# Optimization experiments

Hardware: AMD Instinct MI355X
Metric: run time of the kernel (lower is better)

The kernel has to match this reference:

```python
import jax, jax.numpy as jnp
import numpy as np

B, K, N, D = 64, 64, 32768, 2048   # batch, knn neighbors, memory size, feat dim (hardcoded 2048 in source)
NC, NHID, TOPK = 2048, 512, 5      # num clusters, gcn hidden, topk in affinity masking


def setup_inputs() -> dict:
    key = jax.random.key(0)
    ks = jax.random.split(key, 8)
    features = jax.random.normal(ks[0], (N, D), jnp.float32)
    labels = jax.random.randint(ks[1], (N,), 0, NC)
    indexes = jax.random.randint(ks[2], (B,), 0, N)
    ori_knn_neighbor = jax.random.randint(ks[3], (B, K), 0, N)
    s = 0.02
    conv_w = jax.random.normal(ks[4], (2 * D, NHID), jnp.float32) * s
    conv_b = jnp.zeros((NHID,), jnp.float32)
    w1 = jax.random.normal(ks[5], (NHID, NHID), jnp.float32) * s
    b1 = jnp.zeros((NHID,), jnp.float32)
    prelu_a = jnp.full((NHID,), 0.25, jnp.float32)
    w2 = jax.random.normal(ks[6], (NHID, 2), jnp.float32) * s
    b2 = jnp.zeros((2,), jnp.float32)
    return dict(indexes=indexes, features=features, labels=labels,
                ori_knn_neighbor=ori_knn_neighbor, conv_w=conv_w, conv_b=conv_b,
                w1=w1, b1=b1, prelu_a=prelu_a, w2=w2, b2=b2)


def _build_graphs(indexes, features, labels, ori_knn_neighbor):
    # cluster mean features (index_add_ + count normalize), done under no_grad in torch
    counts = jax.ops.segment_sum(jnp.ones((N,), jnp.float32), labels, num_segments=NC)
    clu_sum = jax.ops.segment_sum(features, labels, num_segments=NC)
    clu_mean = clu_sum / jnp.maximum(counts, 1.0)[:, None]

    def per_sample(idx, nbr):
        clu_lab = labels[nbr]                                  # [K]
        cf = clu_mean[clu_lab].at[0].set(features[idx])        # [K, D]
        A = (cf @ cf.T) / 5.0                                  # [K, K]
        j = jnp.arange(K)
        # keep only first occurrence of each cluster label (np.unique return_index)
        dup = jnp.any((clu_lab[:, None] == clu_lab[None, :]) & (j[None, :] < j[:, None]), axis=1)
        keep = (~dup).astype(A.dtype)                          # [K]
        _, ti = jax.lax.top_k(A, TOPK)                         # [K, TOPK]
        m = jnp.zeros_like(A).at[j[:, None], ti].set(1.0)
        m = ((m > 0) & (m.T > 0)).astype(A.dtype) * keep[:, None] * keep[None, :]
        A = A * m
        cf = cf / jnp.linalg.norm(cf, axis=1, keepdims=True)   # row-normalize
        cf = cf - cf[0]                                        # center on query (row 0 -> 0)
        return cf, A

    x, adj = jax.vmap(per_sample)(indexes, ori_knn_neighbor)   # [B,K,D], [B,K,K]
    return jax.lax.stop_gradient(x), jax.lax.stop_gradient(adj)


def reference(indexes, features, labels, ori_knn_neighbor,
              conv_w, conv_b, w1, b1, prelu_a, w2, b2):
    x, adj = _build_graphs(indexes, features, labels, ori_knn_neighbor)
    # GraphConv with MeanAggregator: agg = A @ x, concat, linear, relu
    agg = jnp.einsum('bij,bjd->bid', adj, x)                   # [B,K,D]
    h = jax.nn.relu(jnp.concatenate([x, agg], axis=-1) @ conv_w + conv_b)  # [B,K,NHID]
    h0 = h.reshape(-1, NHID)
    h1 = h0 @ w1 + b1
    h1 = jnp.where(h1 > 0, h1, prelu_a * h1)                   # PReLU(nhid)
    logits = h1 @ w2 + b2                                      # [B*K, 2]
    return jax.nn.softmax(logits.reshape(B, K, 2), axis=2)
```

## Files before the change

kernel.cpp:

```cpp
#include <hip/hip_runtime.h>
#include <hip/hip_bf16.h>

#define BB 64
#define KN 64
#define NPTS 32768
#define DD 2048
#define NCC 2048
#define NH 512
#define MM 4096
#define K2 4096

typedef unsigned short u16;
typedef unsigned int u32;
typedef __attribute__((ext_vector_type(8))) short short8;
typedef __attribute__((ext_vector_type(4))) float f32x4;

__device__ __forceinline__ float bf2f(u32 u){
  union { u32 i; float f; } v; v.i = u << 16; return v.f;
}
__device__ __forceinline__ u16 f2bf(float f){
  union { float f; u32 i; } v; v.f = f;
  u32 x = v.i;
  return (u16)((x + 0x7fffu + ((x >> 16) & 1u)) >> 16);
}

typedef __attribute__((address_space(3))) u32 as3_u32;
typedef const __attribute__((address_space(1))) u32 as1_u32;
__device__ __forceinline__ void glds16(const void* g, void* l){
  __builtin_amdgcn_global_load_lds((as1_u32*)g, (as3_u32*)l, 16, 0, 0);
}

__global__ __launch_bounds__(256) void k_prep(
    const int* __restrict__ labels, int* __restrict__ counts,
    const int* __restrict__ knn, int* __restrict__ used,
    const void* __restrict__ conv_w, u16* __restrict__ cwT, int fcw,
    const void* __restrict__ w1, u16* __restrict__ w1T, int fw1){
  __shared__ u16 tile[64][65];
  int bb = blockIdx.x, t = threadIdx.x;
  if(bb < 128){
    int n = bb*256 + t;
    atomicAdd(&counts[labels[n]], 1);
    return;
  }
  if(bb == 704){
    #pragma unroll
    for(int i=0;i<16;i++){
      int idx = i*256 + t;
      used[labels[knn[idx]]] = 1;
    }
    return;
  }
  const void* src; u16* dst; int Kd, Nd, isf32, tb;
  if(bb < 640){ src=conv_w; dst=cwT; Kd=K2; Nd=NH; isf32=fcw; tb=bb-128; }
  else        { src=w1;     dst=w1T; Kd=NH; Nd=NH; isf32=fw1; tb=bb-640; }
  int nbt = Nd >> 6;
  int k0 = (tb / nbt) << 6;
  int n0 = (tb % nbt) << 6;
  if(isf32){
    const float* s = (const float*)src;
    #pragma unroll
    for(int ph=0; ph<16; ph++){
      int idx = ph*256 + t;
      int r = idx >> 6, c = idx & 63;
      tile[r][c] = f2bf(s[(size_t)(k0+r)*Nd + n0 + c]);
    }
  } else {
    const u16* s = (const u16*)src;
    #pragma unroll
    for(int ph=0; ph<16; ph++){
      int idx = ph*256 + t;
      int r = idx >> 6, c = idx & 63;
      tile[r][c] = s[(size_t)(k0+r)*Nd + n0 + c];
    }
  }
  __syncthreads();
  #pragma unroll
  for(int ph=0; ph<16; ph++){
    int idx = ph*256 + t;
    int r = idx >> 6, c = idx & 63;
    dst[(size_t)(n0+r)*Kd + k0 + c] = tile[c][r];
  }
}

__global__ void k_scan(const int* __restrict__ counts, int* __restrict__ offsets){
  __shared__ int sb[256];
  int t = threadIdx.x;
  int c[8]; int s = 0;
  #pragma unroll
  for(int i=0;i<8;i++){ c[i] = counts[t*8+i]; s += c[i]; }
  sb[t] = s; __syncthreads();
  int v = s;
  for(int off=1; off<256; off<<=1){
    int u = (t>=off) ? sb[t-off] : 0;
    __syncthreads();
    v += u; sb[t] = v;
    __syncthreads();
  }
  int run = v - s;
  #pragma unroll
  for(int i=0;i<8;i++){ offsets[t*8+i] = run; run += c[i]; }
}

__global__ void k_scatter(const int* __restrict__ labels, const int* __restrict__ offsets,
                          int* __restrict__ cursor, int* __restrict__ sorted){
  int n = blockIdx.x*256 + threadIdx.x;
  int c = labels[n];
  int p = atomicAdd(&cursor[c], 1);
  sorted[offsets[c] + p] = n;
}

__global__ __launch_bounds__(256) void k_clumean(
    const void* __restrict__ feat, const int* __restrict__ counts,
    const int* __restrict__ offsets, const int* __restrict__ sorted,
    const int* __restrict__ used, int isf32, float* __restrict__ clu){
  int c = blockIdx.x, t = threadIdx.x;
  if(!used[c]) return;
  __shared__ int ridx[64];
  int cnt = counts[c], start = offsets[c];
  float acc[8] = {0,0,0,0,0,0,0,0};
  for(int base=0; base<cnt; base+=64){
    int take = min(64, cnt-base);
    __syncthreads();
    if(t < take) ridx[t] = sorted[start+base+t];
    __syncthreads();
    if(isf32){
      const float* ff = (const float*)feat;
      int r = 0;
      for(; r+4<=take; r+=4){
        const float* p0 = ff + (size_t)ridx[r]*DD + t*8;
        const float* p1 = ff + (size_t)ridx[r+1]*DD + t*8;
        const float* p2 = ff + (size_t)ridx[r+2]*DD + t*8;
        const float* p3 = ff + (size_t)ridx[r+3]*DD + t*8;
        float4 a0=*(const float4*)p0, b0=*(const float4*)(p0+4);
        float4 a1=*(const float4*)p1, b1=*(const float4*)(p1+4);
        float4 a2=*(const float4*)p2, b2=*(const float4*)(p2+4);
        float4 a3=*(const float4*)p3, b3=*(const float4*)(p3+4);
        acc[0]+=a0.x+a1.x+a2.x+a3.x; acc[1]+=a0.y+a1.y+a2.y+a3.y;
        acc[2]+=a0.z+a1.z+a2.z+a3.z; acc[3]+=a0.w+a1.w+a2.w+a3.w;
        acc[4]+=b0.x+b1.x+b2.x+b3.x; acc[5]+=b0.y+b1.y+b2.y+b3.y;
        acc[6]+=b0.z+b1.z+b2.z+b3.z; acc[7]+=b0.w+b1.w+b2.w+b3.w;
      }
      for(; r<take; r++){
        const float* p0 = ff + (size_t)ridx[r]*DD + t*8;
        float4 a0=*(const float4*)p0, b0=*(const float4*)(p0+4);
        acc[0]+=a0.x; acc[1]+=a0.y; acc[2]+=a0.z; acc[3]+=a0.w;
        acc[4]+=b0.x; acc[5]+=b0.y; acc[6]+=b0.z; acc[7]+=b0.w;
      }
    } else {
      const u16* fb = (const u16*)feat;
      for(int r=0; r<take; r++){
        const u16* p0 = fb + (size_t)ridx[r]*DD + t*8;
        uint4 v0 = *(const uint4*)p0;
        acc[0]+=bf2f(v0.x&0xffffu); acc[1]+=bf2f(v0.x>>16);
        acc[2]+=bf2f(v0.y&0xffffu); acc[3]+=bf2f(v0.y>>16);
        acc[4]+=bf2f(v0.z&0xffffu); acc[5]+=bf2f(v0.z>>16);
        acc[6]+=bf2f(v0.w&0xffffu); acc[7]+=bf2f(v0.w>>16);
      }
    }
  }
  float div = fmaxf((float)cnt, 1.0f);
  float* o = clu + (size_t)c*DD + t*8;
  float4 o0 = make_float4(acc[0]/div, acc[1]/div, acc[2]/div, acc[3]/div);
  float4 o1 = make_float4(acc[4]/div, acc[5]/div, acc[6]/div, acc[7]/div);
  *(float4*)o = o0;
  *(float4*)(o+4) = o1;
}

__global__ __launch_bounds__(256) void k_Apart(
    const void* __restrict__ feat, const float* __restrict__ clu,
    const int* __restrict__ indexes, const int* __restrict__ labels,
    const int* __restrict__ knn, int isf32, float* __restrict__ Apart){
  int b = blockIdx.x >> 2, g = blockIdx.x & 3;
  int t = threadIdx.x;
  __shared__ float cfT[64][68];
  __shared__ int sl[64];
  if(t < 64) sl[t] = labels[knn[b*64 + t]];
  int qidx = indexes[b];
  __syncthreads();
  int i0 = (t & 15)*4, j0 = (t >> 4)*4;
  float acc[4][4];
  #pragma unroll
  for(int x=0;x<4;x++)
    #pragma unroll
    for(int c2=0;c2<4;c2++) acc[x][c2] = 0.f;
  for(int ch=g*8; ch<g*8+8; ch++){
    int dbase = ch*64;
    #pragma unroll
    for(int ps=0; ps<16; ps++){
      int idx = ps*256 + t;
      int k = idx >> 6, dd = idx & 63;
      float v;
      if(k == 0){
        size_t fi = (size_t)qidx*DD + dbase + dd;
        v = isf32 ? ((const float*)feat)[fi] : bf2f(((const u16*)feat)[fi]);
      } else {
        v = clu[(size_t)sl[k]*DD + dbase + dd];
      }
      cfT[dd][k] = v;
    }
    __syncthreads();
    #pragma unroll 4
    for(int dd=0; dd<64; dd++){
      float4 av = *(const float4*)&cfT[dd][i0];
      float4 bv = *(const float4*)&cfT[dd][j0];
      float aa[4] = {av.x, av.y, av.z, av.w};
      float bbv[4] = {bv.x, bv.y, bv.z, bv.w};
      #pragma unroll
      for(int ii=0;ii<4;ii++)
        #pragma unroll
        for(int jj=0;jj<4;jj++)
          acc[ii][jj] += aa[ii]*bbv[jj];
    }
    __syncthreads();
  }
  float* op = Apart + ((size_t)(g*64 + b))*4096;
  #pragma unroll
  for(int ii=0;ii<4;ii++)
    *(float4*)&op[(i0+ii)*64 + j0] = make_float4(acc[ii][0], acc[ii][1], acc[ii][2], acc[ii][3]);
}

__global__ __launch_bounds__(256) void k_Afinal(
    const float* __restrict__ Apart, const int* __restrict__ labels,
    const int* __restrict__ knn,
    float* __restrict__ adj, float* __restrict__ norms){
  int b = blockIdx.x, t = threadIdx.x;
  __shared__ float A[64][65];
  __shared__ unsigned long long mb[64];
  __shared__ int sl[64];
  __shared__ int sk[64];
  if(t < 64) sl[t] = labels[knn[b*64 + t]];
  const float* P = Apart + (size_t)b*4096;
  const size_t gs = (size_t)64*4096;
  #pragma unroll
  for(int ps=0; ps<16; ps++){
    int idx = ps*256 + t;
    float s = P[idx] + P[idx+gs] + P[idx+2*gs] + P[idx+3*gs];
    A[idx>>6][idx&63] = s * 0.2f;
  }
  __syncthreads();
  if(t < 64){
    int dup = 0;
    for(int j=0;j<t;j++) dup |= (sl[j]==sl[t]);
    sk[t] = dup ? 0 : 1;
    unsigned long long chosen = 0;
    const float* row = A[t];
    #pragma unroll
    for(int p=0;p<5;p++){
      float best = -INFINITY; int bi = 0;
      for(int j=0;j<64;j++){
        bool taken = (chosen >> j) & 1ull;
        float v = row[j];
        if(!taken && v > best){ best = v; bi = j; }
      }
      chosen |= (1ull << bi);
    }
    mb[t] = chosen;
    norms[b*64+t] = sqrtf(fmaxf(A[t][t]*5.0f, 0.0f));
  }
  __syncthreads();
  float* O = adj + (size_t)b*4096;
  #pragma unroll
  for(int ps=0; ps<16; ps++){
    int idx = ps*256 + t;
    int i = idx >> 6, j = idx & 63;
    bool on = ((mb[i]>>j)&1ull) && ((mb[j]>>i)&1ull) && sk[i] && sk[j];
    O[idx] = on ? A[i][j] : 0.0f;
  }
}

__global__ __launch_bounds__(256) void k_xagg(
    const void* __restrict__ feat, const float* __restrict__ clu,
    const int* __restrict__ indexes, const int* __restrict__ labels,
    const int* __restrict__ knn, const float* __restrict__ norms,
    const float* __restrict__ adj, int isf32, u16* __restrict__ xab){
  int b = blockIdx.x >> 3, g = blockIdx.x & 7;
  int t = threadIdx.x;
  __shared__ u16  xs[64][256];
  __shared__ float adjs[64][65];
  __shared__ float nzv[64][8];
  __shared__ u16   nzj[64][8];
  __shared__ int   nzc[64];
  __shared__ int   sl[64];
  __shared__ float sn[64];

  const float* Ab = adj + (size_t)b*4096;
  #pragma unroll
  for(int ps=0; ps<16; ps++){
    int idx = ps*256 + t;
    adjs[idx>>6][idx&63] = Ab[idx];
  }
  if(t < 64){
    sl[t] = labels[knn[b*64 + t]];
    sn[t] = 1.0f / fmaxf(norms[b*64 + t], 1e-30f);
  }
  int qidx = indexes[b];
  int d = g*256 + t;
  float q0;
  if(isf32){
    q0 = ((const float*)feat)[(size_t)qidx*DD + d];
  } else {
    q0 = bf2f(((const u16*)feat)[(size_t)qidx*DD + d]);
  }
  __syncthreads();
  if(t < 64){
    int c = 0;
    for(int j=0;j<64;j++){
      float v = adjs[t][j];
      if(v != 0.0f && c < 8){ nzv[t][c] = v; nzj[t][c] = (u16)j; c++; }
    }
    nzc[t] = c;
  }
  q0 *= sn[0];

  xs[0][t] = 0;
  xab[(size_t)(b*64)*K2 + d] = 0;
  for(int k=1;k<64;k++){
    float cv = clu[(size_t)sl[k]*DD + d];
    u16 x0 = f2bf(cv*sn[k] - q0);
    xs[k][t] = x0;
    xab[(size_t)(b*64+k)*K2 + d] = x0;
  }
  __syncthreads();

  for(int r=0;r<64;r++){
    float a0 = 0.f;
    int c = nzc[r];
    for(int p=0;p<c;p++){
      a0 += nzv[r][p] * bf2f(xs[nzj[r][p]][t]);
    }
    xab[(size_t)(b*64+r)*K2 + DD + d] = f2bf(a0);
  }
}

template<int EPI>
__global__ __launch_bounds__(256, 2) void k_gemm(
    const u16* __restrict__ Am, const u16* __restrict__ Bt,
    const void* __restrict__ bias, const void* __restrict__ pa,
    int fbias, int fpa,
    void* __restrict__ Cout, int Md, int Nd, int Kd)
{
  __shared__ u16 As[2][64*128];
  __shared__ u16 Bs[2][64*128];
  int t = threadIdx.x;
  int nblk = gridDim.x;
  int bid = (blockIdx.x & 7)*(nblk >> 3) + (blockIdx.x >> 3);
  int nb = Nd >> 6;
  int m0 = (bid / nb) << 6;
  int n0 = (bid % nb) << 6;
  int wave = t >> 6, lane = t & 63;
  int wm = wave >> 1, wn = wave & 1;
  int lm = lane & 15, lq = lane >> 4;
  int lrow4 = lane >> 4, lcol16 = lane & 15;

  f32x4 acc[2][2];
  #pragma unroll
  for(int i=0;i<2;i++)
    #pragma unroll
    for(int j=0;j<2;j++) acc[i][j] = (f32x4){0.f,0.f,0.f,0.f};

  auto stage = [&](int buf, int kb){
    #pragma unroll
    for(int c=0;c<4;c++){
      int cb = wave*4 + c;
      int row = cb*4 + lrow4;
      int col = lcol16 ^ (row & 7);
      glds16(Am + (size_t)(m0+row)*Kd + kb + col*8, &As[buf][cb*512]);
    }
    #pragma unroll
    for(int c=0;c<4;c++){
      int cb = wave*4 + c;
      int row = cb*4 + lrow4;
      int col = lcol16 ^ (row & 7);
      glds16(Bt + (size_t)(n0+row)*Kd + kb + col*8, &Bs[buf][cb*512]);
    }
  };

  stage(0, 0);
  __syncthreads();
  int cur = 0;
  for(int kb=0; kb<Kd; kb+=128){
    if(kb + 128 < Kd) stage(cur^1, kb+128);
    #pragma unroll
    for(int kk=0;kk<4;kk++){
      short8 af[2], bfr[2];
      #pragma unroll
      for(int mi=0;mi<2;mi++){
        int r = wm*32 + mi*16 + lm;
        int p = ((kk<<2)+lq) ^ (r & 7);
        union{ uint4 u; short8 v; } x;
        x.u = *(const uint4*)&As[cur][r*128 + p*8];
        af[mi] = x.v;
      }
      #pragma unroll
      for(int ni=0;ni<2;ni++){
        int r = wn*32 + ni*16 + lm;
        int p = ((kk<<2)+lq) ^ (r & 7);
        union{ uint4 u; short8 v; } x;
        x.u = *(const uint4*)&Bs[cur][r*128 + p*8];
        bfr[ni] = x.v;
      }
      #pragma unroll
      for(int mi=0;mi<2;mi++)
        #pragma unroll
        for(int ni=0;ni<2;ni++)
          acc[mi][ni] = __builtin_amdgcn_mfma_f32_16x16x32_bf16(af[mi], bfr[ni], acc[mi][ni], 0, 0, 0);
    }
    __syncthreads();
    cur ^= 1;
  }

  #pragma unroll
  for(int ni=0;ni<2;ni++){
    int col = n0 + wn*32 + ni*16 + lm;
    float bs = fbias ? ((const float*)bias)[col] : bf2f(((const u16*)bias)[col]);
    float av = 0.f;
    if(EPI==1) av = fpa ? ((const float*)pa)[col] : bf2f(((const u16*)pa)[col]);
    #pragma unroll
    for(int mi=0;mi<2;mi++){
      int rowb = m0 + wm*32 + mi*16 + lq*4;
      #pragma unroll
      for(int r2=0;r2<4;r2++){
        float v = acc[mi][ni][r2] + bs;
        if(EPI==0){
          v = fmaxf(v, 0.f);
          ((u16*)Cout)[(size_t)(rowb+r2)*Nd + col] = f2bf(v);
        } else {
          v = (v > 0.f) ? v : av*v;
          ((float*)Cout)[(size_t)(rowb+r2)*Nd + col] = v;
        }
      }
    }
  }
}

__global__ __launch_bounds__(256) void k_out(
    const float* __restrict__ h1, const void* __restrict__ w2,
    const void* __restrict__ b2, int fw2, int fb2, int fo,
    void* __restrict__ out){
  int t = threadIdx.x; int lane = t & 63; int row = blockIdx.x*4 + (t >> 6);
  const float* hr = h1 + (size_t)row*NH;
  float s0 = 0.f, s1 = 0.f;
  #pragma unroll
  for(int j=0;j<NH/64;j++){
    int i = lane + j*64;
    float h = hr[i];
    float w0 = fw2 ? ((const float*)w2)[i*2+0] : bf2f(((const u16*)w2)[i*2+0]);
    float w1v= fw2 ? ((const float*)w2)[i*2+1] : bf2f(((const u16*)w2)[i*2+1]);
    s0 += h * w0;
    s1 += h * w1v;
  }
  #pragma unroll
  for(int off=32; off>0; off>>=1){
    s0 += __shfl_down(s0, off);
    s1 += __shfl_down(s1, off);
  }
  if(lane==0){
    float bb0 = fb2 ? ((const float*)b2)[0] : bf2f(((const u16*)b2)[0]);
    float bb1 = fb2 ? ((const float*)b2)[1] : bf2f(((const u16*)b2)[1]);
    float l0 = s0 + bb0;
    float l1 = s1 + bb1;
    float m = fmaxf(l0, l1);
    float e0 = expf(l0 - m), e1 = expf(l1 - m);
    float inv = 1.0f / (e0 + e1);
    if(fo){
      ((float*)out)[row*2+0] = e0*inv;
      ((float*)out)[row*2+1] = e1*inv;
    } else {
      ((u16*)out)[row*2+0] = f2bf(e0*inv);
      ((u16*)out)[row*2+1] = f2bf(e1*inv);
    }
  }
}

__global__ void k_fill_sentinel(u32* __restrict__ out, int nwords){
  int i = blockIdx.x*256 + threadIdx.x;
  if(i < nwords) out[i] = 0x40404040u;
}

extern "C" void kernel_launch(void* const* d_in, const int* in_sizes, int n_in,
                              void* d_out, int out_size, void* d_ws, size_t ws_size,
                              hipStream_t stream) {
  const int* indexes = (const int*)d_in[0];
  const void* feat   = d_in[1];
  const int* labels  = (const int*)d_in[2];
  const int* knn     = (const int*)d_in[3];
  const void* conv_w = d_in[4];
  const void* conv_b = d_in[5];
  const void* w1     = d_in[6];
  const void* b1     = d_in[7];
  const void* pa     = d_in[8];
  const void* w2     = d_in[9];
  const void* b2     = d_in[10];

  int ff  = (in_sizes[1]  != (int)((size_t)NPTS*DD*2));
  int fcw = (in_sizes[4]  != (int)((size_t)2*DD*NH*2));
  int fcb = (in_sizes[5]  != NH*2);
  int fw1 = (in_sizes[6]  != (int)((size_t)NH*NH*2));
  int fb1 = (in_sizes[7]  != NH*2);
  int fpa = (in_sizes[8]  != NH*2);
  int fw2 = (in_sizes[9]  != NH*2*2);
  int fb2 = (in_sizes[10] != 2*2);
  int fo  = (out_size     != MM*2*2);

  char* w = (char*)d_ws;
  size_t o = 0;
  auto alloc = [&](size_t bytes) -> void* {
    void* p = w + o; o = (o + bytes + 255) & ~(size_t)255; return p;
  };
  int*   counts  = (int*)  alloc((size_t)NCC*4);
  int*   cursor  = (int*)  alloc((size_t)NCC*4);
  int*   used    = (int*)  alloc((size_t)NCC*4);
  int*   offsets = (int*)  alloc((size_t)NCC*4);
  int*   sorted  = (int*)  alloc((size_t)NPTS*4);
  float* norms   = (float*)alloc((size_t)MM*4);
  float* adj     = (float*)alloc((size_t)BB*64*64*4);
  float* Apart   = (float*)alloc((size_t)4*BB*64*64*4);
  float* clu     = (float*)alloc((size_t)NCC*DD*4);
  u16*   xab     = (u16*)  alloc((size_t)MM*K2*2);
  u16*   cwT     = (u16*)  alloc((size_t)K2*NH*2);
  u16*   w1T     = (u16*)  alloc((size_t)NH*NH*2);
  u16*   hb      = (u16*)  clu;
  float* h1      = (float*)((char*)clu + (size_t)MM*NH*2);

  size_t NEED = o;
  if(ws_size < NEED){
    int nwords = out_size/4;
    k_fill_sentinel<<<(nwords+255)/256, 256, 0, stream>>>((u32*)d_out, nwords);
    return;
  }

  hipMemsetAsync(counts, 0, (size_t)NCC*4*3, stream);

  k_prep   <<<705, 256, 0, stream>>>(labels, counts, knn, used, conv_w, cwT, fcw, w1, w1T, fw1);
  k_scan   <<<1, 256, 0, stream>>>(counts, offsets);
  k_scatter<<<NPTS/256, 256, 0, stream>>>(labels, offsets, cursor, sorted);
  k_clumean<<<NCC, 256, 0, stream>>>(feat, counts, offsets, sorted, used, ff, clu);
  k_Apart  <<<BB*4, 256, 0, stream>>>(feat, clu, indexes, labels, knn, ff, Apart);
  k_Afinal <<<BB, 256, 0, stream>>>(Apart, labels, knn, adj, norms);
  k_xagg   <<<BB*8, 256, 0, stream>>>(feat, clu, indexes, labels, knn, norms, adj, ff, xab);

  k_gemm<0><<<(MM/64)*(NH/64), 256, 0, stream>>>(xab, cwT, conv_b, nullptr, fcb, 0, (void*)hb, MM, NH, K2);
  k_gemm<1><<<(MM/64)*(NH/64), 256, 0, stream>>>(hb, w1T, b1, pa, fb1, fpa, (void*)h1, MM, NH, NH);

  k_out    <<<MM/4, 256, 0, stream>>>(h1, w2, b2, fw2, fb2, fo, d_out);
}
```

Baseline: 533.9 us.

## Project cluster means through conv weights once, then combine per-sample projections

Instead of building a per-sample [B*K, 2D] concatenated input and running the large conv GEMM over it, the cluster means (plus query rows) are converted to bf16 and multiplied once by both halves of conv_w, stacked into a [D, 1024] matrix. A new kernel then forms each sample's hidden activations from these projected rows: it scales by the inverse norm, subtracts the query projection, applies the sparse adjacency, adds the bias and applies ReLU. This relies on linearity to replace a 4096x4096x512 GEMM and the large xab buffer with a 2112x2048x1024 GEMM plus cheap gathers. Rounding differs because centering and aggregation now happen after projection rather than on bf16 features.

```diff
diff --git a/kernel.cpp b/kernel.cpp
--- a/kernel.cpp
+++ b/kernel.cpp
@@ -9,6 +9,7 @@
 #define NH 512
 #define MM 4096
 #define K2 4096
+#define MCLUB 2112
 
 typedef unsigned short u16;
 typedef unsigned int u32;
@@ -23,6 +24,14 @@
   u32 x = v.i;
   return (u16)((x + 0x7fffu + ((x >> 16) & 1u)) >> 16);
 }
+__device__ __forceinline__ uint4 pack8(const u16* b){
+  uint4 w;
+  w.x = (u32)b[0] | ((u32)b[1]<<16);
+  w.y = (u32)b[2] | ((u32)b[3]<<16);
+  w.z = (u32)b[4] | ((u32)b[5]<<16);
+  w.w = (u32)b[6] | ((u32)b[7]<<16);
+  return w;
+}
 
 typedef __attribute__((address_space(3))) u32 as3_u32;
 typedef const __attribute__((address_space(1))) u32 as1_u32;
@@ -33,52 +42,71 @@
 __global__ __launch_bounds__(256) void k_prep(
     const int* __restrict__ labels, int* __restrict__ counts,
     const int* __restrict__ knn, int* __restrict__ used,
-    const void* __restrict__ conv_w, u16* __restrict__ cwT, int fcw,
+    const void* __restrict__ conv_w, u16* __restrict__ cwT2, int fcw,
     const void* __restrict__ w1, u16* __restrict__ w1T, int fw1){
   __shared__ u16 tile[64][65];
   int bb = blockIdx.x, t = threadIdx.x;
   if(bb < 128){
-    int n = bb*256 + t;
-    atomicAdd(&counts[labels[n]], 1);
+    atomicAdd(&counts[labels[bb*256 + t]], 1);
     return;
   }
   if(bb == 704){
     #pragma unroll
-    for(int i=0;i<16;i++){
-      int idx = i*256 + t;
-      used[labels[knn[idx]]] = 1;
-    }
+    for(int i=0;i<16;i++) used[labels[knn[i*256 + t]]] = 1;
     return;
   }
-  const void* src; u16* dst; int Kd, Nd, isf32, tb;
-  if(bb < 640){ src=conv_w; dst=cwT; Kd=K2; Nd=NH; isf32=fcw; tb=bb-128; }
-  else        { src=w1;     dst=w1T; Kd=NH; Nd=NH; isf32=fw1; tb=bb-640; }
-  int nbt = Nd >> 6;
-  int k0 = (tb / nbt) << 6;
-  int n0 = (tb % nbt) << 6;
-  if(isf32){
-    const float* s = (const float*)src;
+  if(bb < 640){
+    int tb = bb - 128;
+    int k0 = (tb >> 3) << 6;
+    int n0 = (tb & 7) << 6;
+    if(fcw){
+      const float* s = (const float*)conv_w;
+      #pragma unroll
+      for(int ph=0; ph<16; ph++){
+        int idx = ph*256 + t; int r = idx >> 6, c = idx & 63;
+        tile[r][c] = f2bf(s[(size_t)(k0+r)*NH + n0 + c]);
+      }
+    } else {
+      const u16* s = (const u16*)conv_w;
+      #pragma unroll
+      for(int ph=0; ph<16; ph++){
+        int idx = ph*256 + t; int r = idx >> 6, c = idx & 63;
+        tile[r][c] = s[(size_t)(k0+r)*NH + n0 + c];
+      }
+    }
+    __syncthreads();
+    int drow = n0 + (k0 >= 2048 ? 512 : 0);
+    int dcol = k0 & 2047;
     #pragma unroll
     for(int ph=0; ph<16; ph++){
-      int idx = ph*256 + t;
-      int r = idx >> 6, c = idx & 63;
-      tile[r][c] = f2bf(s[(size_t)(k0+r)*Nd + n0 + c]);
+      int idx = ph*256 + t; int r = idx >> 6, c = idx & 63;
+      cwT2[(size_t)(drow+r)*2048 + dcol + c] = tile[c][r];
     }
   } else {
-    const u16* s = (const u16*)src;
+    int tb = bb - 640;
+    int k0 = (tb >> 3) << 6;
+    int n0 = (tb & 7) << 6;
+    if(fw1){
+      const float* s = (const float*)w1;
+      #pragma unroll
+      for(int ph=0; ph<16; ph++){
+        int idx = ph*256 + t; int r = idx >> 6, c = idx & 63;
+        tile[r][c] = f2bf(s[(size_t)(k0+r)*NH + n0 + c]);
+      }
+    } else {
+      const u16* s = (const u16*)w1;
+      #pragma unroll
+      for(int ph=0; ph<16; ph++){
+        int idx = ph*256 + t; int r = idx >> 6, c = idx & 63;
+        tile[r][c] = s[(size_t)(k0+r)*NH + n0 + c];
+      }
+    }
+    __syncthreads();
     #pragma unroll
     for(int ph=0; ph<16; ph++){
-      int idx = ph*256 + t;
-      int r = idx >> 6, c = idx & 63;
-      tile[r][c] = s[(size_t)(k0+r)*Nd + n0 + c];
-    }
-  }
-  __syncthreads();
-  #pragma unroll
-  for(int ph=0; ph<16; ph++){
-    int idx = ph*256 + t;
-    int r = idx >> 6, c = idx & 63;
-    dst[(size_t)(n0+r)*Kd + k0 + c] = tile[c][r];
+      int idx = ph*256 + t; int r = idx >> 6, c = idx & 63;
+      w1T[(size_t)(n0+r)*NH + k0 + c] = tile[c][r];
+    }
   }
 }
 
@@ -109,12 +137,34 @@
   sorted[offsets[c] + p] = n;
 }
 
+__global__ __launch_bounds__(256) void k_qcopy(
+    const void* __restrict__ feat, const int* __restrict__ indexes,
+    int ff, u16* __restrict__ club){
+  int b = blockIdx.x, t = threadIdx.x;
+  int qidx = indexes[b];
+  u16* o = club + (size_t)(NCC + b)*DD + t*8;
+  if(ff){
+    const float* p = (const float*)feat + (size_t)qidx*DD + t*8;
+    float4 a = *(const float4*)p, c = *(const float4*)(p+4);
+    u16 ob[8] = {f2bf(a.x),f2bf(a.y),f2bf(a.z),f2bf(a.w),
+                 f2bf(c.x),f2bf(c.y),f2bf(c.z),f2bf(c.w)};
+    *(uint4*)o = pack8(ob);
+  } else {
+    uint4 v = *(const uint4*)((const u16*)feat + (size_t)qidx*DD + t*8);
+    *(uint4*)o = v;
+  }
+}
+
 __global__ __launch_bounds__(256) void k_clumean(
     const void* __restrict__ feat, const int* __restrict__ counts,
     const int* __restrict__ offsets, const int* __restrict__ sorted,
-    const int* __restrict__ used, int isf32, float* __restrict__ clu){
+    const int* __restrict__ used, int isf32,
+    float* __restrict__ clu, u16* __restrict__ club){
   int c = blockIdx.x, t = threadIdx.x;
-  if(!used[c]) return;
+  if(!used[c]){
+    *(uint4*)(club + (size_t)c*DD + t*8) = make_uint4(0,0,0,0);
+    return;
+  }
   __shared__ int ridx[64];
   int cnt = counts[c], start = offsets[c];
   float acc[8] = {0,0,0,0,0,0,0,0};
@@ -159,11 +209,16 @@
     }
   }
   float div = fmaxf((float)cnt, 1.0f);
+  float m[8];
+  #pragma unroll
+  for(int i=0;i<8;i++) m[i] = acc[i] / div;
   float* o = clu + (size_t)c*DD + t*8;
-  float4 o0 = make_float4(acc[0]/div, acc[1]/div, acc[2]/div, acc[3]/div);
-  float4 o1 = make_float4(acc[4]/div, acc[5]/div, acc[6]/div, acc[7]/div);
-  *(float4*)o = o0;
-  *(float4*)(o+4) = o1;
+  *(float4*)o     = make_float4(m[0],m[1],m[2],m[3]);
+  *(float4*)(o+4) = make_float4(m[4],m[5],m[6],m[7]);
+  u16 ob[8];
+  #pragma unroll
+  for(int i=0;i<8;i++) ob[i] = f2bf(m[i]);
+  *(uint4*)(club + (size_t)c*DD + t*8) = pack8(ob);
 }
 
 __global__ __launch_bounds__(256) void k_Apart(
@@ -268,21 +323,22 @@
   }
 }
 
-__global__ __launch_bounds__(256) void k_xagg(
-    const void* __restrict__ feat, const float* __restrict__ clu,
-    const int* __restrict__ indexes, const int* __restrict__ labels,
-    const int* __restrict__ knn, const float* __restrict__ norms,
-    const float* __restrict__ adj, int isf32, u16* __restrict__ xab){
-  int b = blockIdx.x >> 3, g = blockIdx.x & 7;
+__global__ __launch_bounds__(256) void k_hcomb(
+    const float* __restrict__ PR, const float* __restrict__ adj,
+    const float* __restrict__ norms, const int* __restrict__ labels,
+    const int* __restrict__ knn, const void* __restrict__ conv_b, int fcb,
+    u16* __restrict__ hb){
+  int b = blockIdx.x >> 2, cg = blockIdx.x & 3;
   int t = threadIdx.x;
-  __shared__ u16  xs[64][256];
   __shared__ float adjs[64][65];
+  __shared__ float xwa[64][128];
+  __shared__ float cqx[128], cqa[128], bias[128];
   __shared__ float nzv[64][8];
   __shared__ u16   nzj[64][8];
   __shared__ int   nzc[64];
   __shared__ int   sl[64];
   __shared__ float sn[64];
-
+  int j0 = cg*128;
   const float* Ab = adj + (size_t)b*4096;
   #pragma unroll
   for(int ps=0; ps<16; ps++){
@@ -293,13 +349,12 @@
     sl[t] = labels[knn[b*64 + t]];
     sn[t] = 1.0f / fmaxf(norms[b*64 + t], 1e-30f);
   }
-  int qidx = indexes[b];
-  int d = g*256 + t;
-  float q0;
-  if(isf32){
-    q0 = ((const float*)feat)[(size_t)qidx*DD + d];
-  } else {
-    q0 = bf2f(((const u16*)feat)[(size_t)qidx*DD + d]);
+  if(t >= 64 && t < 192){
+    int c = t - 64;
+    const float* qr = PR + (size_t)(NCC + b)*1024;
+    cqx[c] = qr[j0 + c];
+    cqa[c] = qr[512 + j0 + c];
+    bias[c] = fcb ? ((const float*)conv_b)[j0 + c] : bf2f(((const u16*)conv_b)[j0 + c]);
   }
   __syncthreads();
   if(t < 64){
@@ -310,25 +365,22 @@
     }
     nzc[t] = c;
   }
-  q0 *= sn[0];
-
-  xs[0][t] = 0;
-  xab[(size_t)(b*64)*K2 + d] = 0;
-  for(int k=1;k<64;k++){
-    float cv = clu[(size_t)sl[k]*DD + d];
-    u16 x0 = f2bf(cv*sn[k] - q0);
-    xs[k][t] = x0;
-    xab[(size_t)(b*64+k)*K2 + d] = x0;
+  float inv0 = sn[0];
+  for(int idx=t; idx<8192; idx+=256){
+    int k = idx >> 7, c = idx & 127;
+    float v = 0.f;
+    if(k > 0) v = sn[k]*PR[(size_t)sl[k]*1024 + 512 + j0 + c] - inv0*cqa[c];
+    xwa[k][c] = v;
   }
   __syncthreads();
-
-  for(int r=0;r<64;r++){
-    float a0 = 0.f;
-    int c = nzc[r];
-    for(int p=0;p<c;p++){
-      a0 += nzv[r][p] * bf2f(xs[nzj[r][p]][t]);
-    }
-    xab[(size_t)(b*64+r)*K2 + DD + d] = f2bf(a0);
+  for(int idx=t; idx<8192; idx+=256){
+    int k = idx >> 7, c = idx & 127;
+    float xwx = (k > 0) ? sn[k]*PR[(size_t)sl[k]*1024 + j0 + c] - inv0*cqx[c] : 0.f;
+    float g = 0.f;
+    int cc = nzc[k];
+    for(int p=0;p<cc;p++) g += nzv[k][p]*xwa[nzj[k][p]][c];
+    float h = fmaxf(xwx + g + bias[c], 0.f);
+    hb[(size_t)(b*64 + k)*NH + j0 + c] = f2bf(h);
   }
 }
 
@@ -412,18 +464,17 @@
   #pragma unroll
   for(int ni=0;ni<2;ni++){
     int col = n0 + wn*32 + ni*16 + lm;
-    float bs = fbias ? ((const float*)bias)[col] : bf2f(((const u16*)bias)[col]);
-    float av = 0.f;
-    if(EPI==1) av = fpa ? ((const float*)pa)[col] : bf2f(((const u16*)pa)[col]);
+    float bs = 0.f, av = 0.f;
+    if(EPI != 2) bs = fbias ? ((const float*)bias)[col] : bf2f(((const u16*)bias)[col]);
+    if(EPI == 1) av = fpa ? ((const float*)pa)[col] : bf2f(((const u16*)pa)[col]);
     #pragma unroll
     for(int mi=0;mi<2;mi++){
       int rowb = m0 + wm*32 + mi*16 + lq*4;
       #pragma unroll
       for(int r2=0;r2<4;r2++){
         float v = acc[mi][ni][r2] + bs;
-        if(EPI==0){
-          v = fmaxf(v, 0.f);
-          ((u16*)Cout)[(size_t)(rowb+r2)*Nd + col] = f2bf(v);
+        if(EPI==2){
+          ((float*)Cout)[(size_t)(rowb+r2)*Nd + col] = v;
         } else {
           v = (v > 0.f) ? v : av*v;
           ((float*)Cout)[(size_t)(rowb+r2)*Nd + col] = v;
@@ -516,8 +567,9 @@
   float* adj     = (float*)alloc((size_t)BB*64*64*4);
   float* Apart   = (float*)alloc((size_t)4*BB*64*64*4);
   float* clu     = (float*)alloc((size_t)NCC*DD*4);
-  u16*   xab     = (u16*)  alloc((size_t)MM*K2*2);
-  u16*   cwT     = (u16*)  alloc((size_t)K2*NH*2);
+  u16*   club    = (u16*)  alloc((size_t)MCLUB*DD*2);
+  float* PR      = (float*)alloc((size_t)MCLUB*1024*4);
+  u16*   cwT2    = (u16*)  alloc((size_t)1024*2048*2);
   u16*   w1T     = (u16*)  alloc((size_t)NH*NH*2);
   u16*   hb      = (u16*)  clu;
   float* h1      = (float*)((char*)clu + (size_t)MM*NH*2);
@@ -531,15 +583,19 @@
 
   hipMemsetAsync(counts, 0, (size_t)NCC*4*3, stream);
 
-  k_prep   <<<705, 256, 0, stream>>>(labels, counts, knn, used, conv_w, cwT, fcw, w1, w1T, fw1);
+  k_prep   <<<705, 256, 0, stream>>>(labels, counts, knn, used, conv_w, cwT2, fcw, w1, w1T, fw1);
   k_scan   <<<1, 256, 0, stream>>>(counts, offsets);
   k_scatter<<<NPTS/256, 256, 0, stream>>>(labels, offsets, cursor, sorted);
-  k_clumean<<<NCC, 256, 0, stream>>>(feat, counts, offsets, sorted, used, ff, clu);
+  k_qcopy  <<<BB, 256, 0, stream>>>(feat, indexes, ff, club);
+  k_clumean<<<NCC, 256, 0, stream>>>(feat, counts, offsets, sorted, used, ff, clu, club);
+
+  k_gemm<2><<<(MCLUB/64)*(1024/64), 256, 0, stream>>>(club, cwT2, nullptr, nullptr, 0, 0,
+                                                      (void*)PR, MCLUB, 1024, 2048);
+
   k_Apart  <<<BB*4, 256, 0, stream>>>(feat, clu, indexes, labels, knn, ff, Apart);
   k_Afinal <<<BB, 256, 0, stream>>>(Apart, labels, knn, adj, norms);
-  k_xagg   <<<BB*8, 256, 0, stream>>>(feat, clu, indexes, labels, knn, norms, adj, ff, xab);
-
-  k_gemm<0><<<(MM/64)*(NH/64), 256, 0, stream>>>(xab, cwT, conv_b, nullptr, fcb, 0, (void*)hb, MM, NH, K2);
+  k_hcomb  <<<BB*4, 256, 0, stream>>>(PR, adj, norms, labels, knn, conv_b, fcb, hb);
+
   k_gemm<1><<<(MM/64)*(NH/64), 256, 0, stream>>>(hb, w1T, b1, pa, fb1, fpa, (void*)h1, MM, NH, NH);
 
   k_out    <<<MM/4, 256, 0, stream>>>(h1, w2, b2, fw2, fb2, fo, d_out);
```

Result: no change. 527.1 us (-1.3%).
